# Optimization experiments

Measured on AMD Instinct MI355X. Metric: run time of the kernel, lower is better.

The kernel has to match this reference:

```python
import jax, jax.numpy as jnp
import numpy as np

NUM_BITS = 4
BLOCK = 64
IN_F = 4096
OUT_F = 4096
RANK = 16


def dequantize(packed_qweight, weight_max, lookup_table):
    """Unpack sub-byte indices from uint8 bytes, lookup codebook, apply per-block absmax scale.
    packed_qweight: [n_bytes, 1] uint8; weight_max: [n_blocks]; lookup_table: [2**NUM_BITS].
    Returns dequantized weight [OUT_F, IN_F]."""
    nipb = 8 // NUM_BITS  # indices per byte
    mask = (1 << NUM_BITS) - 1
    b = packed_qweight[:, 0]
    # index i was packed at bit position i*NUM_BITS (LSB first)
    idx = jnp.stack([(b >> (i * NUM_BITS)) & mask for i in range(nipb)], axis=-1).reshape(-1)
    w = lookup_table[idx].reshape(-1, BLOCK) * weight_max[:, None]  # [n_blocks, BLOCK]
    return w.reshape(OUT_F, IN_F)


def setup_inputs() -> dict:
    key = jax.random.key(0)
    k0, k1, k2, k3, k4, k5 = jax.random.split(key, 6)
    x = jax.random.normal(k0, (4, 2048, IN_F), dtype=jnp.float32)
    packed_qweight = jax.random.randint(k1, (OUT_F * IN_F // (8 // NUM_BITS), 1), 0, 256, dtype=jnp.int32).astype(jnp.uint8)
    weight_max = jax.random.uniform(k2, (OUT_F * IN_F // BLOCK,), dtype=jnp.float32, minval=0.01, maxval=0.1)
    # uniform non-symmetric codebook: linspace(-1, 1, 2**num_bits)
    lookup_table = jnp.linspace(-1.0, 1.0, 2 ** NUM_BITS, dtype=jnp.float32)
    lora_A = jax.random.normal(k3, (RANK, IN_F), dtype=jnp.float32) * 0.02
    lora_B = jax.random.normal(k4, (OUT_F, RANK), dtype=jnp.float32) * 0.02
    bias = jax.random.normal(k5, (OUT_F,), dtype=jnp.float32) * 0.02
    return {"x": x, "packed_qweight": packed_qweight, "weight_max": weight_max,
            "lookup_table": lookup_table, "lora_A": lora_A, "lora_B": lora_B, "bias": bias}


def reference(x, packed_qweight, weight_max, lookup_table, lora_A, lora_B, bias):
    W = dequantize(packed_qweight, weight_max, lookup_table)  # [OUT_F, IN_F]
    base = jnp.einsum('bsi,oi->bso', x, W)
    lora = jnp.einsum('bsr,or->bso', jnp.einsum('bsi,ri->bsr', x, lora_A), lora_B)
    return base + lora + bias
```

## Files before the change

### kernel.cpp

```cpp
#include <hip/hip_runtime.h>
#include <hip/hip_bf16.h>
#include <stdint.h>

constexpr int IN_F  = 4096;
constexpr int OUT_F = 4096;
constexpr int M_ROWS = 4 * 2048;
constexpr int RANK = 16;

typedef short short8 __attribute__((ext_vector_type(8)));
typedef float f32x4 __attribute__((ext_vector_type(4)));

__device__ __forceinline__ short f2bf(float f) {
  return __builtin_bit_cast(short, __float2bfloat16(f));
}

__device__ __forceinline__ void gload16(const void* g, void* l) {
  __builtin_amdgcn_global_load_lds(
      (const __attribute__((address_space(1))) void*)g,
      (__attribute__((address_space(3))) void*)l, 16, 0, 0);
}

__global__ __launch_bounds__(256) void prep_kernel(
    const int* __restrict__ q,
    const float* __restrict__ wmax,
    const float* __restrict__ lut,
    const float* __restrict__ lA,
    const float* __restrict__ lB,
    const float* __restrict__ x,
    __hip_bfloat16* __restrict__ W,
    __hip_bfloat16* __restrict__ xb) {
  if (blockIdx.x < 512) {
    __shared__ float slut[16];
    if (threadIdx.x < 16) slut[threadIdx.x] = lut[threadIdx.x];
    __syncthreads();

    const int bx = blockIdx.x & 7, by = blockIdx.x >> 3;
    const int o0  = by * 64 + (threadIdx.x >> 5) * 8;
    const int ib0 = bx * 512 + (threadIdx.x & 31) * 16;

    #pragma unroll
    for (int h = 0; h < 2; ++h) {
      const int ib = ib0 + h * 8;
      float w[8][8];
      #pragma unroll
      for (int p = 0; p < 8; ++p) {
        const size_t l = (size_t)(o0 + p) * IN_F + ib;
        const int4 u = *(const int4*)(q + (l >> 1));
        const float sc = wmax[l >> 6];
        w[p][0] = slut[u.x & 15] * sc;
        w[p][1] = slut[(u.x >> 4) & 15] * sc;
        w[p][2] = slut[u.y & 15] * sc;
        w[p][3] = slut[(u.y >> 4) & 15] * sc;
        w[p][4] = slut[u.z & 15] * sc;
        w[p][5] = slut[(u.z >> 4) & 15] * sc;
        w[p][6] = slut[u.w & 15] * sc;
        w[p][7] = slut[(u.w >> 4) & 15] * sc;
      }
      #pragma unroll 2
      for (int r = 0; r < 16; ++r) {
        const float* ar = lA + (size_t)r * IN_F + ib;
        const float4 a0 = *(const float4*)(ar);
        const float4 a1 = *(const float4*)(ar + 4);
        float b[8];
        #pragma unroll
        for (int p = 0; p < 8; ++p) b[p] = lB[(size_t)(o0 + p) * RANK + r];
        #pragma unroll
        for (int p = 0; p < 8; ++p) {
          w[p][0] += b[p] * a0.x; w[p][1] += b[p] * a0.y;
          w[p][2] += b[p] * a0.z; w[p][3] += b[p] * a0.w;
          w[p][4] += b[p] * a1.x; w[p][5] += b[p] * a1.y;
          w[p][6] += b[p] * a1.z; w[p][7] += b[p] * a1.w;
        }
      }
      #pragma unroll
      for (int p = 0; p < 8; ++p) {
        short8 s;
        #pragma unroll
        for (int qq = 0; qq < 8; ++qq) s[qq] = f2bf(w[p][qq]);
        *(short8*)&W[(size_t)(o0 + p) * IN_F + ib] = s;
      }
    }
  } else {
    constexpr int NG = (M_ROWS * IN_F) / 8;
    const int nblk = 2048;
    const int stride = nblk * 256;
    for (int i = (blockIdx.x - 512) * 256 + threadIdx.x; i < NG; i += stride) {
      const float4 a = ((const float4*)x)[2 * i];
      const float4 b = ((const float4*)x)[2 * i + 1];
      short8 s;
      s[0] = f2bf(a.x); s[1] = f2bf(a.y); s[2] = f2bf(a.z); s[3] = f2bf(a.w);
      s[4] = f2bf(b.x); s[5] = f2bf(b.y); s[6] = f2bf(b.z); s[7] = f2bf(b.w);
      ((short8*)xb)[i] = s;
    }
  }
}

constexpr int BM = 256, BN = 256, BK = 64;
constexpr int GM = M_ROWS, GN = OUT_F, GK = IN_F;
constexpr int NKT = GK / BK;

#define LOAD_B(BUF, KH)                                                   \
  _Pragma("unroll")                                                       \
  for (int n_ = 0; n_ < 4; ++n_)                                          \
    bf[n_] = *(const short8*)&sB[BUF][KH][wn * 64 + n_ * 16 + lr][swr * 8];

#define LOAD_A(BUF, KH, MH)                                               \
  _Pragma("unroll")                                                       \
  for (int i_ = 0; i_ < 4; ++i_)                                          \
    af[i_] = *(const short8*)&sA[BUF][KH][wm * 128 + (MH) * 64 + i_ * 16 + lr][swr * 8];

#define MFMA_Q(MH)                                                        \
  __builtin_amdgcn_s_setprio(1);                                          \
  _Pragma("unroll")                                                       \
  for (int i_ = 0; i_ < 4; ++i_)                                          \
    _Pragma("unroll")                                                     \
    for (int n_ = 0; n_ < 4; ++n_)                                        \
      acc[(MH) * 4 + i_][n_] = __builtin_amdgcn_mfma_f32_16x16x32_bf16(   \
          af[i_], bf[n_], acc[(MH) * 4 + i_][n_], 0, 0, 0);               \
  __builtin_amdgcn_s_setprio(0);

#define PHASE(BUF, KH, MH, DOB, GB, LB, VM)                               \
  do {                                                                    \
    if (VM) asm volatile("s_waitcnt vmcnt(6)" ::: "memory");              \
    __builtin_amdgcn_s_barrier();                                         \
    stage(GB, LB);                                                        \
    if (DOB) { LOAD_B(BUF, KH) }                                          \
    LOAD_A(BUF, KH, MH)                                                   \
    MFMA_Q(MH)                                                            \
    __builtin_amdgcn_sched_barrier(0);                                    \
  } while (0)

__global__ __launch_bounds__(512, 2) void gemm_bt_1bar(
    const __hip_bfloat16* __restrict__ A,
    const __hip_bfloat16* __restrict__ B,
    const float* __restrict__ bias,
    float* __restrict__ C) {
  __shared__ __hip_bfloat16 sA[2][2][256][32];
  __shared__ __hip_bfloat16 sB[2][2][256][32];

  const int tid  = threadIdx.x;
  const int lane = tid & 63;
  const int wave = tid >> 6;
  const int lr = lane & 15;
  const int lk = lane >> 4;
  const int wm = wave >> 2;
  const int wn = wave & 3;
  const int swr = lk ^ ((lr >> 1) & 3);

  const int bid = blockIdx.x;
  const int cpx = gridDim.x >> 3;
  const int wg  = (bid & 7) * cpx + (bid >> 3);
  const int nbn = GN / BN;
  const int m0 = (wg / nbn) * BM;
  const int n0 = (wg % nbn) * BN;

  const __hip_bfloat16* Abase = A + (size_t)m0 * GK;
  const __hip_bfloat16* Bbase = B + (size_t)n0 * GK;

  const int swst = (tid >> 3) & 3;
  auto stage = [&](const __hip_bfloat16* gb, __hip_bfloat16* lb) {
    #pragma unroll
    for (int j = 0; j < 2; ++j) {
      const int c = j * 512 + tid;
      const int row = c >> 2, slot = c & 3;
      const int sg = slot ^ swst;
      gload16(gb + (size_t)row * GK + sg * 8,
              (void*)((char*)lb + (j * 512 + wave * 64) * 16));
    }
  };

  f32x4 acc[8][4];
  #pragma unroll
  for (int m = 0; m < 8; ++m)
    #pragma unroll
    for (int n = 0; n < 4; ++n) acc[m][n] = (f32x4)0.0f;

  stage(Abase +  0, &sA[0][0][0][0]);
  stage(Bbase +  0, &sB[0][0][0][0]);
  stage(Abase + 32, &sA[0][1][0][0]);
  stage(Bbase + 32, &sB[0][1][0][0]);
  stage(Bbase + 64, &sB[1][0][0][0]);
  stage(Abase + 64, &sA[1][0][0][0]);
  stage(Bbase + 96, &sB[1][1][0][0]);
  asm volatile("s_waitcnt vmcnt(6)" ::: "memory");

  short8 af[4], bf[4];

  for (int t = 0; t < NKT; t += 2) {
    const int t2 = (t + 2 < NKT) ? t + 2 : NKT - 1;
    const int t3 = (t + 3 < NKT) ? t + 3 : NKT - 1;

    PHASE(0, 0, 0, true,  Abase + (size_t)(t + 1) * 64 + 32, &sA[1][1][0][0], false);
    PHASE(0, 0, 1, false, Bbase + (size_t)t2 * 64,           &sB[0][0][0][0], false);
    PHASE(0, 1, 0, true,  Abase + (size_t)t2 * 64,           &sA[0][0][0][0], false);
    PHASE(0, 1, 1, false, Bbase + (size_t)t2 * 64 + 32,      &sB[0][1][0][0], true);
    PHASE(1, 0, 0, true,  Abase + (size_t)t2 * 64 + 32,      &sA[0][1][0][0], false);
    PHASE(1, 0, 1, false, Bbase + (size_t)t3 * 64,           &sB[1][0][0][0], false);
    PHASE(1, 1, 0, true,  Abase + (size_t)t3 * 64,           &sA[1][0][0][0], false);
    PHASE(1, 1, 1, false, Bbase + (size_t)t3 * 64 + 32,      &sB[1][1][0][0], true);
  }

  #pragma unroll
  for (int n = 0; n < 4; ++n) {
    const int col = n0 + wn * 64 + n * 16 + lr;
    const float bv = bias[col];
    #pragma unroll
    for (int m = 0; m < 8; ++m) {
      const int row = m0 + wm * 128 + m * 16 + lk * 4;
      #pragma unroll
      for (int j = 0; j < 4; ++j)
        C[(size_t)(row + j) * GN + col] = acc[m][n][j] + bv;
    }
  }
}

extern "C" void kernel_launch(void* const* d_in, const int* in_sizes, int n_in,
                              void* d_out, int out_size, void* d_ws, size_t ws_size,
                              hipStream_t stream) {
  const float* x    = (const float*)d_in[0];
  const int*   qw   = (const int*)d_in[1];
  const float* wmax = (const float*)d_in[2];
  const float* lut  = (const float*)d_in[3];
  const float* lA   = (const float*)d_in[4];
  const float* lB   = (const float*)d_in[5];
  const float* bias = (const float*)d_in[6];
  float* out = (float*)d_out;

  __hip_bfloat16* Weff = (__hip_bfloat16*)d_ws;
  __hip_bfloat16* xb   = (__hip_bfloat16*)((char*)d_ws + (size_t)OUT_F * IN_F * 2);

  prep_kernel<<<2560, 256, 0, stream>>>(qw, wmax, lut, lA, lB, x, Weff, xb);
  gemm_bt_1bar<<<(GM / BM) * (GN / BN), 512, 0, stream>>>(xb, Weff, bias, out);
}
```

Before: 323.4 us.

## Replace 256x256 eight-phase GEMM with simpler 256x128 double-buffered tile kernel

Result: slower. 346.4 us (+7.1%).

```diff
diff --git a/kernel.cpp b/kernel.cpp
--- a/kernel.cpp
+++ b/kernel.cpp
@@ -82,8 +82,7 @@
     }
   } else {
     constexpr int NG = (M_ROWS * IN_F) / 8;
-    const int nblk = 2048;
-    const int stride = nblk * 256;
+    const int stride = 2048 * 256;
     for (int i = (blockIdx.x - 512) * 256 + threadIdx.x; i < NG; i += stride) {
       const float4 a = ((const float4*)x)[2 * i];
       const float4 b = ((const float4*)x)[2 * i + 1];
@@ -95,56 +94,25 @@
   }
 }
 
-constexpr int BM = 256, BN = 256, BK = 64;
+constexpr int BM = 256, BN = 128, BK = 32;
 constexpr int GM = M_ROWS, GN = OUT_F, GK = IN_F;
 constexpr int NKT = GK / BK;
 
-#define LOAD_B(BUF, KH)                                                   \
-  _Pragma("unroll")                                                       \
-  for (int n_ = 0; n_ < 4; ++n_)                                          \
-    bf[n_] = *(const short8*)&sB[BUF][KH][wn * 64 + n_ * 16 + lr][swr * 8];
-
-#define LOAD_A(BUF, KH, MH)                                               \
-  _Pragma("unroll")                                                       \
-  for (int i_ = 0; i_ < 4; ++i_)                                          \
-    af[i_] = *(const short8*)&sA[BUF][KH][wm * 128 + (MH) * 64 + i_ * 16 + lr][swr * 8];
-
-#define MFMA_Q(MH)                                                        \
-  __builtin_amdgcn_s_setprio(1);                                          \
-  _Pragma("unroll")                                                       \
-  for (int i_ = 0; i_ < 4; ++i_)                                          \
-    _Pragma("unroll")                                                     \
-    for (int n_ = 0; n_ < 4; ++n_)                                        \
-      acc[(MH) * 4 + i_][n_] = __builtin_amdgcn_mfma_f32_16x16x32_bf16(   \
-          af[i_], bf[n_], acc[(MH) * 4 + i_][n_], 0, 0, 0);               \
-  __builtin_amdgcn_s_setprio(0);
-
-#define PHASE(BUF, KH, MH, DOB, GB, LB, VM)                               \
-  do {                                                                    \
-    if (VM) asm volatile("s_waitcnt vmcnt(6)" ::: "memory");              \
-    __builtin_amdgcn_s_barrier();                                         \
-    stage(GB, LB);                                                        \
-    if (DOB) { LOAD_B(BUF, KH) }                                          \
-    LOAD_A(BUF, KH, MH)                                                   \
-    MFMA_Q(MH)                                                            \
-    __builtin_amdgcn_sched_barrier(0);                                    \
-  } while (0)
-
-__global__ __launch_bounds__(512, 2) void gemm_bt_1bar(
+__global__ __launch_bounds__(256, 2) void gemm_bt_2blk(
     const __hip_bfloat16* __restrict__ A,
     const __hip_bfloat16* __restrict__ B,
     const float* __restrict__ bias,
     float* __restrict__ C) {
-  __shared__ __hip_bfloat16 sA[2][2][256][32];
-  __shared__ __hip_bfloat16 sB[2][2][256][32];
+  __shared__ __hip_bfloat16 sA[2][256][32];
+  __shared__ __hip_bfloat16 sB[2][128][32];
 
   const int tid  = threadIdx.x;
   const int lane = tid & 63;
   const int wave = tid >> 6;
   const int lr = lane & 15;
   const int lk = lane >> 4;
-  const int wm = wave >> 2;
-  const int wn = wave & 3;
+  const int wm = wave >> 1;
+  const int wn = wave & 1;
   const int swr = lk ^ ((lr >> 1) & 3);
 
   const int bid = blockIdx.x;
@@ -158,14 +126,22 @@
   const __hip_bfloat16* Bbase = B + (size_t)n0 * GK;
 
   const int swst = (tid >> 3) & 3;
-  auto stage = [&](const __hip_bfloat16* gb, __hip_bfloat16* lb) {
-    #pragma unroll
-    for (int j = 0; j < 2; ++j) {
-      const int c = j * 512 + tid;
+  auto stageA = [&](const __hip_bfloat16* gb, __hip_bfloat16* lb) {
+    #pragma unroll
+    for (int k = 0; k < 4; ++k) {
+      const int c = k * 256 + tid;
       const int row = c >> 2, slot = c & 3;
-      const int sg = slot ^ swst;
-      gload16(gb + (size_t)row * GK + sg * 8,
-              (void*)((char*)lb + (j * 512 + wave * 64) * 16));
+      gload16(gb + (size_t)row * GK + (size_t)((slot ^ swst) * 8),
+              (void*)((char*)lb + (k * 256 + wave * 64) * 16));
+    }
+  };
+  auto stageB = [&](const __hip_bfloat16* gb, __hip_bfloat16* lb) {
+    #pragma unroll
+    for (int k = 0; k < 2; ++k) {
+      const int c = k * 256 + tid;
+      const int row = c >> 2, slot = c & 3;
+      gload16(gb + (size_t)row * GK + (size_t)((slot ^ swst) * 8),
+              (void*)((char*)lb + (k * 256 + wave * 64) * 16));
     }
   };
 
@@ -175,29 +151,35 @@
     #pragma unroll
     for (int n = 0; n < 4; ++n) acc[m][n] = (f32x4)0.0f;
 
-  stage(Abase +  0, &sA[0][0][0][0]);
-  stage(Bbase +  0, &sB[0][0][0][0]);
-  stage(Abase + 32, &sA[0][1][0][0]);
-  stage(Bbase + 32, &sB[0][1][0][0]);
-  stage(Bbase + 64, &sB[1][0][0][0]);
-  stage(Abase + 64, &sA[1][0][0][0]);
-  stage(Bbase + 96, &sB[1][1][0][0]);
-  asm volatile("s_waitcnt vmcnt(6)" ::: "memory");
-
-  short8 af[4], bf[4];
-
-  for (int t = 0; t < NKT; t += 2) {
-    const int t2 = (t + 2 < NKT) ? t + 2 : NKT - 1;
-    const int t3 = (t + 3 < NKT) ? t + 3 : NKT - 1;
-
-    PHASE(0, 0, 0, true,  Abase + (size_t)(t + 1) * 64 + 32, &sA[1][1][0][0], false);
-    PHASE(0, 0, 1, false, Bbase + (size_t)t2 * 64,           &sB[0][0][0][0], false);
-    PHASE(0, 1, 0, true,  Abase + (size_t)t2 * 64,           &sA[0][0][0][0], false);
-    PHASE(0, 1, 1, false, Bbase + (size_t)t2 * 64 + 32,      &sB[0][1][0][0], true);
-    PHASE(1, 0, 0, true,  Abase + (size_t)t2 * 64 + 32,      &sA[0][1][0][0], false);
-    PHASE(1, 0, 1, false, Bbase + (size_t)t3 * 64,           &sB[1][0][0][0], false);
-    PHASE(1, 1, 0, true,  Abase + (size_t)t3 * 64,           &sA[1][0][0][0], false);
-    PHASE(1, 1, 1, false, Bbase + (size_t)t3 * 64 + 32,      &sB[1][1][0][0], true);
+  stageA(Abase, &sA[0][0][0]);
+  stageB(Bbase, &sB[0][0][0]);
+
+  for (int t = 0; t < NKT; ++t) {
+    const int buf = t & 1;
+    const int tn = (t + 1 < NKT) ? t + 1 : t;
+    stageA(Abase + (size_t)tn * BK, &sA[buf ^ 1][0][0]);
+    stageB(Bbase + (size_t)tn * BK, &sB[buf ^ 1][0][0]);
+    asm volatile("s_waitcnt vmcnt(6)" ::: "memory");
+    __builtin_amdgcn_s_barrier();
+
+    short8 af[8], bf[4];
+    #pragma unroll
+    for (int n = 0; n < 4; ++n)
+      bf[n] = *(const short8*)&sB[buf][wn * 64 + n * 16 + lr][swr * 8];
+    #pragma unroll
+    for (int m = 0; m < 8; ++m)
+      af[m] = *(const short8*)&sA[buf][wm * 128 + m * 16 + lr][swr * 8];
+
+    __builtin_amdgcn_s_setprio(1);
+    #pragma unroll
+    for (int m = 0; m < 8; ++m)
+      #pragma unroll
+      for (int n = 0; n < 4; ++n)
+        acc[m][n] = __builtin_amdgcn_mfma_f32_16x16x32_bf16(
+            af[m], bf[n], acc[m][n], 0, 0, 0);
+    __builtin_amdgcn_s_setprio(0);
+    __builtin_amdgcn_sched_barrier(0);
+    __builtin_amdgcn_s_barrier();
   }
 
   #pragma unroll
@@ -230,5 +212,5 @@
   __hip_bfloat16* xb   = (__hip_bfloat16*)((char*)d_ws + (size_t)OUT_F * IN_F * 2);
 
   prep_kernel<<<2560, 256, 0, stream>>>(qw, wmax, lut, lA, lB, x, Weff, xb);
-  gemm_bt_1bar<<<(GM / BM) * (GN / BN), 512, 0, stream>>>(xb, Weff, bias, out);
-}
+  gemm_bt_2blk<<<(GM / BM) * (GN / BN), 256, 0, stream>>>(xb, Weff, bias, out);
+}
```

## Switch GEMM to 32x32x16 MFMA tiles and restructure phase synchronization

Applied to the files above, without the earlier changes.

Measured after the change: 341.1 us. +5.5%, slower.

```diff
diff --git a/kernel.cpp b/kernel.cpp
--- a/kernel.cpp
+++ b/kernel.cpp
@@ -8,7 +8,7 @@
 constexpr int RANK = 16;
 
 typedef short short8 __attribute__((ext_vector_type(8)));
-typedef float f32x4 __attribute__((ext_vector_type(4)));
+typedef float f32x16 __attribute__((ext_vector_type(16)));
 
 __device__ __forceinline__ short f2bf(float f) {
   return __builtin_bit_cast(short, __float2bfloat16(f));
@@ -82,8 +82,7 @@
     }
   } else {
     constexpr int NG = (M_ROWS * IN_F) / 8;
-    const int nblk = 2048;
-    const int stride = nblk * 256;
+    const int stride = 2048 * 256;
     for (int i = (blockIdx.x - 512) * 256 + threadIdx.x; i < NG; i += stride) {
       const float4 a = ((const float4*)x)[2 * i];
       const float4 b = ((const float4*)x)[2 * i + 1];
@@ -99,38 +98,45 @@
 constexpr int GM = M_ROWS, GN = OUT_F, GK = IN_F;
 constexpr int NKT = GK / BK;
 
-#define LOAD_B(BUF, KH)                                                   \
+#define LOAD_B32(BUF, KH)                                                 \
   _Pragma("unroll")                                                       \
-  for (int n_ = 0; n_ < 4; ++n_)                                          \
-    bf[n_] = *(const short8*)&sB[BUF][KH][wn * 64 + n_ * 16 + lr][swr * 8];
-
-#define LOAD_A(BUF, KH, MH)                                               \
+  for (int nt_ = 0; nt_ < 2; ++nt_)                                       \
+    _Pragma("unroll")                                                     \
+    for (int ks_ = 0; ks_ < 2; ++ks_)                                     \
+      bf[nt_][ks_] = *(const short8*)&sB[BUF][KH][wn * 64 + nt_ * 32 + l31][(((ks_ * 2 + lhi) ^ swz) * 8)];
+
+#define LOAD_A32(BUF, KH, MH)                                             \
   _Pragma("unroll")                                                       \
-  for (int i_ = 0; i_ < 4; ++i_)                                          \
-    af[i_] = *(const short8*)&sA[BUF][KH][wm * 128 + (MH) * 64 + i_ * 16 + lr][swr * 8];
-
-#define MFMA_Q(MH)                                                        \
+  for (int mt_ = 0; mt_ < 2; ++mt_)                                       \
+    _Pragma("unroll")                                                     \
+    for (int ks_ = 0; ks_ < 2; ++ks_)                                     \
+      af[mt_][ks_] = *(const short8*)&sA[BUF][KH][wm * 128 + (MH) * 64 + mt_ * 32 + l31][(((ks_ * 2 + lhi) ^ swz) * 8)];
+
+#define MFMA_Q32(MH)                                                      \
   __builtin_amdgcn_s_setprio(1);                                          \
   _Pragma("unroll")                                                       \
-  for (int i_ = 0; i_ < 4; ++i_)                                          \
+  for (int mt_ = 0; mt_ < 2; ++mt_)                                       \
     _Pragma("unroll")                                                     \
-    for (int n_ = 0; n_ < 4; ++n_)                                        \
-      acc[(MH) * 4 + i_][n_] = __builtin_amdgcn_mfma_f32_16x16x32_bf16(   \
-          af[i_], bf[n_], acc[(MH) * 4 + i_][n_], 0, 0, 0);               \
+    for (int nt_ = 0; nt_ < 2; ++nt_)                                     \
+      _Pragma("unroll")                                                   \
+      for (int ks_ = 0; ks_ < 2; ++ks_)                                   \
+        acc[(MH) * 2 + mt_][nt_] = __builtin_amdgcn_mfma_f32_32x32x16_bf16( \
+            af[mt_][ks_], bf[nt_][ks_], acc[(MH) * 2 + mt_][nt_], 0, 0, 0); \
   __builtin_amdgcn_s_setprio(0);
 
 #define PHASE(BUF, KH, MH, DOB, GB, LB, VM)                               \
   do {                                                                    \
+    if (DOB) { LOAD_B32(BUF, KH) }                                        \
+    LOAD_A32(BUF, KH, MH)                                                 \
+    stage(GB, LB);                                                        \
     if (VM) asm volatile("s_waitcnt vmcnt(6)" ::: "memory");              \
     __builtin_amdgcn_s_barrier();                                         \
-    stage(GB, LB);                                                        \
-    if (DOB) { LOAD_B(BUF, KH) }                                          \
-    LOAD_A(BUF, KH, MH)                                                   \
-    MFMA_Q(MH)                                                            \
+    MFMA_Q32(MH)                                                          \
     __builtin_amdgcn_sched_barrier(0);                                    \
+    __builtin_amdgcn_s_barrier();                                         \
   } while (0)
 
-__global__ __launch_bounds__(512, 2) void gemm_bt_1bar(
+__global__ __launch_bounds__(512, 2) void gemm_bt_32x32(
     const __hip_bfloat16* __restrict__ A,
     const __hip_bfloat16* __restrict__ B,
     const float* __restrict__ bias,
@@ -141,11 +147,11 @@
   const int tid  = threadIdx.x;
   const int lane = tid & 63;
   const int wave = tid >> 6;
-  const int lr = lane & 15;
-  const int lk = lane >> 4;
+  const int l31 = lane & 31;
+  const int lhi = lane >> 5;
   const int wm = wave >> 2;
   const int wn = wave & 3;
-  const int swr = lk ^ ((lr >> 1) & 3);
+  const int swz = (l31 >> 1) & 3;
 
   const int bid = blockIdx.x;
   const int cpx = gridDim.x >> 3;
@@ -169,11 +175,11 @@
     }
   };
 
-  f32x4 acc[8][4];
+  f32x16 acc[4][2];
   #pragma unroll
-  for (int m = 0; m < 8; ++m)
-    #pragma unroll
-    for (int n = 0; n < 4; ++n) acc[m][n] = (f32x4)0.0f;
+  for (int m = 0; m < 4; ++m)
+    #pragma unroll
+    for (int n = 0; n < 2; ++n) acc[m][n] = (f32x16)0.0f;
 
   stage(Abase +  0, &sA[0][0][0][0]);
   stage(Bbase +  0, &sB[0][0][0][0]);
@@ -183,8 +189,9 @@
   stage(Abase + 64, &sA[1][0][0][0]);
   stage(Bbase + 96, &sB[1][1][0][0]);
   asm volatile("s_waitcnt vmcnt(6)" ::: "memory");
-
-  short8 af[4], bf[4];
+  __builtin_amdgcn_s_barrier();
+
+  short8 af[2][2], bf[2][2];
 
   for (int t = 0; t < NKT; t += 2) {
     const int t2 = (t + 2 < NKT) ? t + 2 : NKT - 1;
@@ -201,15 +208,17 @@
   }
 
   #pragma unroll
-  for (int n = 0; n < 4; ++n) {
-    const int col = n0 + wn * 64 + n * 16 + lr;
+  for (int nt = 0; nt < 2; ++nt) {
+    const int col = n0 + wn * 64 + nt * 32 + l31;
     const float bv = bias[col];
     #pragma unroll
-    for (int m = 0; m < 8; ++m) {
-      const int row = m0 + wm * 128 + m * 16 + lk * 4;
+    for (int amt = 0; amt < 4; ++amt) {
+      const int rb = m0 + wm * 128 + amt * 32 + 4 * lhi;
       #pragma unroll
-      for (int j = 0; j < 4; ++j)
-        C[(size_t)(row + j) * GN + col] = acc[m][n][j] + bv;
+      for (int reg = 0; reg < 16; ++reg) {
+        const int row = rb + (reg & 3) + 8 * (reg >> 2);
+        C[(size_t)row * GN + col] = acc[amt][nt][reg] + bv;
+      }
     }
   }
 }
@@ -230,5 +239,5 @@
   __hip_bfloat16* xb   = (__hip_bfloat16*)((char*)d_ws + (size_t)OUT_F * IN_F * 2);
 
   prep_kernel<<<2560, 256, 0, stream>>>(qw, wmax, lut, lA, lB, x, Weff, xb);
-  gemm_bt_1bar<<<(GM / BM) * (GN / BN), 512, 0, stream>>>(xb, Weff, bias, out);
-}
+  gemm_bt_32x32<<<(GM / BM) * (GN / BN), 512, 0, stream>>>(xb, Weff, bias, out);
+}
```
